# Optimization experiments

Hardware: AMD Instinct MI355X
Metric: run time of the kernel (lower is better)

Reference implementation:

```python
import jax, jax.numpy as jnp
import numpy as np

B, C, H, W = 32, 64, 64, 64
OC = 2 * C  # same_c=False -> out_channels = 2*in_channels


def _conv(x, w, b, stride):
    y = jax.lax.conv_general_dilated(
        x, w, (stride, stride), ((1, 1), (1, 1)),
        dimension_numbers=('NCHW', 'OIHW', 'NCHW'))
    return y + b[None, :, None, None]


def _lrelu(x):
    return jnp.where(x >= 0, x, 0.1 * x)


def _roi_align_full(x, ph, pw, sr=2):
    # torchvision RoIAlign, aligned=False, spatial_scale=1, sampling_ratio=2,
    # single ROI per batch item covering [0, 0, W-1, H-1].
    b, c, h, w = x.shape
    bin_h = max(float(h - 1), 1.0) / ph
    bin_w = max(float(w - 1), 1.0) / pw
    off = (jnp.arange(sr, dtype=jnp.float32) + 0.5) / sr
    ys = ((jnp.arange(ph, dtype=jnp.float32)[:, None] + off[None, :]).reshape(-1) * bin_h)  # [ph*sr]
    xs = ((jnp.arange(pw, dtype=jnp.float32)[:, None] + off[None, :]).reshape(-1) * bin_w)  # [pw*sr]
    y0 = jnp.floor(ys).astype(jnp.int32)
    x0 = jnp.floor(xs).astype(jnp.int32)
    y1 = jnp.minimum(y0 + 1, h - 1)
    x1 = jnp.minimum(x0 + 1, w - 1)
    ly = ys - y0.astype(jnp.float32); hy = 1.0 - ly
    lx = xs - x0.astype(jnp.float32); hx = 1.0 - lx
    # gather 4 bilinear corners: [B, C, ph*sr, pw*sr]
    v00 = x[:, :, y0][:, :, :, x0]
    v01 = x[:, :, y0][:, :, :, x1]
    v10 = x[:, :, y1][:, :, :, x0]
    v11 = x[:, :, y1][:, :, :, x1]
    val = (hy[:, None] * hx[None, :]) * v00 + (hy[:, None] * lx[None, :]) * v01 \
        + (ly[:, None] * hx[None, :]) * v10 + (ly[:, None] * lx[None, :]) * v11
    # average the sr x sr samples per bin
    return val.reshape(b, c, ph, sr, pw, sr).mean(axis=(3, 5))


def setup_inputs() -> dict:
    key = jax.random.key(0)
    ks = jax.random.split(key, 20)
    def p(k, shape):
        return jax.random.normal(k, shape, dtype=jnp.float32) * 0.05
    return {
        'out1': jax.random.normal(ks[0], (B, C, H, W), dtype=jnp.float32),
        'out2': jax.random.normal(ks[1], (B, C, H, W), dtype=jnp.float32),
        'out3': jax.random.normal(ks[2], (B, C, H, W), dtype=jnp.float32),
        'w1': p(ks[3], (OC, C, 3, 3)),      'b1': p(ks[4], (OC,)),
        'w2': p(ks[5], (OC, OC, 3, 3)),     'b2': p(ks[6], (OC,)),
        'w3': p(ks[7], (OC, OC, 3, 3)),     'b3': p(ks[8], (OC,)),
        'w_aux': p(ks[9], (OC, OC, 3, 3)),  'b_aux': p(ks[10], (OC,)),
        'w_b2': p(ks[11], (OC, 2 * OC, 3, 3)), 'b_b2': p(ks[12], (OC,)),
        'w_prev': p(ks[13], (OC, 2 * C, 3, 3)), 'b_prev': p(ks[14], (OC,)),
        'lin_w': p(ks[15], (H * W, C)),     'lin_b': p(ks[16], (H * W,)),
    }


def reference(out1, out2, out3, w1, b1, w2, b2, w3, b3,
              w_aux, b_aux, w_b2, b_b2, w_prev, b_prev, lin_w, lin_b):
    bsz, c, h, w = out1.shape
    l1 = _lrelu(_conv(out1, w1, b1, 1))
    l2 = _lrelu(_conv(l1, w2, b2, 1))
    l3 = _lrelu(_conv(l2, w3, b3, 1))
    roi1 = _roi_align_full(l2, h // 2, w // 2)
    aux = _lrelu(_conv(l3, w_aux, b_aux, 2))        # dropout = identity (eval)
    block_out1 = roi1 + aux
    block_out2 = _lrelu(_conv(jnp.concatenate([l1, l2], axis=1), w_b2, b_b2, 2))
    prev = _lrelu(_conv(jnp.concatenate([out2, out3], axis=1), w_prev, b_prev, 1))
    # fused per-pixel attention: logits[b,p] = <lin_w[p], out1[b,:,p]> + lin_b[p]
    xp = out1.reshape(bsz, c, h * w)                 # [B, C, P], P row-major over (h, w)
    logits = jnp.einsum('bcp,pc->bp', xp, lin_w) + lin_b
    attn = jax.nn.softmax(logits, axis=-1).reshape(bsz, 1, h, w)
    block_out3 = _roi_align_full(prev * attn, h // 2, w // 2)
    return jnp.stack([block_out1 + block_out2 + block_out3, block_out2, block_out3])
```

## Files before the change

### kernel.cpp

```cpp
#include <hip/hip_runtime.h>
#include <hip/hip_bf16.h>

typedef __attribute__((ext_vector_type(8))) short short8;
typedef __attribute__((ext_vector_type(4))) float f32x4;

constexpr int B = 32, C = 64, HW = 4096;

__device__ __forceinline__ unsigned short f2bf(float f) {
    __hip_bfloat16 h = __float2bfloat16(f);
    unsigned short u; __builtin_memcpy(&u, &h, 2); return u;
}
__device__ __forceinline__ float b2f(unsigned short u) {
    unsigned int t = ((unsigned int)u) << 16; float f; __builtin_memcpy(&f, &t, 4); return f;
}
__device__ __forceinline__ void gllds16(const void* g, void* l) {
    __builtin_amdgcn_global_load_lds((const __attribute__((address_space(1))) unsigned int*)g,
                                     (__attribute__((address_space(3))) unsigned int*)l, 16, 0, 0);
}

__global__ __launch_bounds__(256) void tr_k(const float* __restrict__ out1,
                                            const float* __restrict__ out2,
                                            const float* __restrict__ out3,
                                            unsigned short* __restrict__ t1,
                                            unsigned short* __restrict__ tp)
{
    int t = threadIdx.x;
    int px = blockIdx.x * 256 + t;
    int b = blockIdx.y;
    if (blockIdx.z == 0) {
        const float* src = out1 + (size_t)b * 64 * HW + px;
        unsigned short v[64];
#pragma unroll
        for (int c = 0; c < 64; ++c) v[c] = f2bf(src[(size_t)c * HW]);
        unsigned short* dst = t1 + ((size_t)b * HW + px) * 64;
#pragma unroll
        for (int j = 0; j < 8; ++j)
            *(short8*)(dst + j * 8) = *(short8*)(v + j * 8);
    } else {
        const float* s2 = out2 + (size_t)b * 64 * HW + px;
        const float* s3 = out3 + (size_t)b * 64 * HW + px;
        unsigned short v[128];
#pragma unroll
        for (int c = 0; c < 64; ++c) v[c] = f2bf(s2[(size_t)c * HW]);
#pragma unroll
        for (int c = 0; c < 64; ++c) v[64 + c] = f2bf(s3[(size_t)c * HW]);
        unsigned short* dst = tp + ((size_t)b * HW + px) * 128;
#pragma unroll
        for (int j = 0; j < 16; ++j)
            *(short8*)(dst + j * 8) = *(short8*)(v + j * 8);
    }
}

__global__ __launch_bounds__(256) void logits_k(const float* __restrict__ out1,
                                                const float* __restrict__ lin_w,
                                                const float* __restrict__ lin_b,
                                                float* __restrict__ logits)
{
    int b = blockIdx.x >> 4;
    int p = (blockIdx.x & 15) * 256 + threadIdx.x;
    float acc = lin_b[p];
    const float* xb = out1 + (size_t)b * C * HW + p;
    const float* wp = lin_w + (size_t)p * C;
#pragma unroll
    for (int c = 0; c < C; c += 4) {
        float4 w4 = *(const float4*)(wp + c);
        acc = fmaf(xb[(size_t)c * HW],       w4.x, acc);
        acc = fmaf(xb[(size_t)(c + 1) * HW], w4.y, acc);
        acc = fmaf(xb[(size_t)(c + 2) * HW], w4.z, acc);
        acc = fmaf(xb[(size_t)(c + 3) * HW], w4.w, acc);
    }
    logits[(size_t)b * HW + p] = acc;
}

__global__ __launch_bounds__(256) void softmax_k(const float* __restrict__ logits,
                                                 float* __restrict__ attn)
{
    int b = blockIdx.x, tid = threadIdx.x;
    float lg[16];
#pragma unroll
    for (int k = 0; k < 16; ++k) lg[k] = logits[(size_t)b * HW + tid + (k << 8)];
    __shared__ float red[256];
    float m = -INFINITY;
#pragma unroll
    for (int k = 0; k < 16; ++k) m = fmaxf(m, lg[k]);
    red[tid] = m; __syncthreads();
    for (int s = 128; s > 0; s >>= 1) {
        if (tid < s) red[tid] = fmaxf(red[tid], red[tid + s]);
        __syncthreads();
    }
    m = red[0]; __syncthreads();
    float se = 0.f;
#pragma unroll
    for (int k = 0; k < 16; ++k) { lg[k] = __expf(lg[k] - m); se += lg[k]; }
    red[tid] = se; __syncthreads();
    for (int s = 128; s > 0; s >>= 1) {
        if (tid < s) red[tid] += red[tid + s];
        __syncthreads();
    }
    float inv = 1.0f / red[0];
#pragma unroll
    for (int k = 0; k < 16; ++k)
        attn[(size_t)b * HW + tid + (k << 8)] = lg[k] * inv;
}

__global__ __launch_bounds__(256) void wprep_k(const float* w1, const float* w2, const float* w3,
                                               const float* wa, const float* wb2, const float* wp,
                                               unsigned short* __restrict__ wT)
{
    int blk = blockIdx.x;
    int base, ic, l2ic, off; const float* src;
    if      (blk < 32)  { base = 0;   ic = 64;  l2ic = 6; off = 0;      src = w1;  }
    else if (blk < 96)  { base = 32;  ic = 128; l2ic = 7; off = 73728;  src = w2;  }
    else if (blk < 160) { base = 96;  ic = 128; l2ic = 7; off = 221184; src = w3;  }
    else if (blk < 224) { base = 160; ic = 128; l2ic = 7; off = 368640; src = wa;  }
    else if (blk < 352) { base = 224; ic = 256; l2ic = 8; off = 516096; src = wb2; }
    else                { base = 352; ic = 128; l2ic = 7; off = 811008; src = wp;  }
    int pair = (blk - base) * 256 + threadIdx.x;
    int oc = pair >> l2ic, icx = pair & (ic - 1);
    const float* s = src + ((size_t)(oc * ic + icx)) * 9;
#pragma unroll
    for (int k = 0; k < 9; ++k)
        wT[(size_t)off + ((size_t)(k * 128 + oc)) * ic + icx] = f2bf(s[k]);
}

template<int IC, int STRIDE, int PS_IN, int CO_IN, int OPS, int OCO, bool ATTN>
__global__ __launch_bounds__(256, 4) void conv_k(
    const unsigned short* __restrict__ in,
    const unsigned short* __restrict__ wTc,
    const float* __restrict__ bias,
    const float* __restrict__ attn,
    unsigned short* __restrict__ out)
{
    constexpr int NICG = IC / 32;
    constexpr int L = (IC == 64) ? 1 : (IC == 128) ? 2 : 3;
    constexpr int NS = 9 * NICG;
    constexpr int NPX = (STRIDE == 1) ? 4096 : 1024;
    constexpr int WO = (STRIDE == 1) ? 64 : 32;

    __shared__ char bsm[2][8192];

    int t = threadIdx.x;
    int wave = t >> 6, lane = t & 63;
    int mw = wave & 1, nw = wave >> 1;
    int l15 = lane & 15, lc = lane >> 4;
    int y0 = blockIdx.x, b = blockIdx.y;

    int bofs[4];
#pragma unroll
    for (int nf = 0; nf < 4; ++nf) {
        int oc = nw * 64 + nf * 16 + l15;
        bofs[nf] = oc * 64 + ((lc ^ ((oc >> 1) & 3)) << 4);
    }
    int oc0 = t >> 2;
    int c0 = (t & 3) ^ ((oc0 >> 1) & 3);
    const unsigned short* wsrc = wTc + oc0 * IC + c0 * 8;
    char* lbase = &bsm[0][0] + (wave << 10);

    const unsigned short* base_b = in + (size_t)b * HW * PS_IN + CO_IN + (lc << 3);
    int col[2];
#pragma unroll
    for (int f = 0; f < 2; ++f)
        col[f] = (STRIDE == 1) ? (mw * 32 + f * 16 + l15) : (f * 16 + l15);

    f32x4 acc[2][4];
#pragma unroll
    for (int f = 0; f < 2; ++f)
#pragma unroll
        for (int nf = 0; nf < 4; ++nf) acc[f][nf] = (f32x4)0.0f;

    auto stage = [&](int s, int buf) {
        int kk = s >> L, icg = s & (NICG - 1);
        const unsigned short* p = wsrc + (size_t)kk * 128 * IC + icg * 32;
        char* d = lbase + buf * 8192;
        gllds16(p, d);
        gllds16(p + 64 * IC, d + 4096);
    };

    stage(0, 0);
    __syncthreads();

    for (int s = 0; s < NS; ++s) {
        int cur = s & 1;
        if (s + 1 < NS) stage(s + 1, cur ^ 1);
        int kk = s >> L, icg = s & (NICG - 1);
        int ky = (kk * 11) >> 5;
        int kx = kk - ky * 3;
        int iy = (STRIDE == 1) ? (y0 + ky - 1) : ((y0 * 2 + mw) * 2 + ky - 1);
        bool yok = (unsigned)iy < 64u;
        const unsigned short* prow = base_b + (long)iy * (64 * PS_IN) + icg * 32;
        short8 az = {0, 0, 0, 0, 0, 0, 0, 0};
        short8 aa[2];
#pragma unroll
        for (int f = 0; f < 2; ++f) {
            int ix = (STRIDE == 1) ? (col[f] + kx - 1) : (2 * col[f] + kx - 1);
            bool ok = yok && ((unsigned)ix < 64u);
            const short8* ap = (const short8*)(prow + (long)ix * PS_IN);
            aa[f] = ok ? *ap : az;
        }
        const char* bb_base = &bsm[0][0] + cur * 8192;
        short8 bb[4];
#pragma unroll
        for (int nf = 0; nf < 4; ++nf)
            bb[nf] = *(const short8*)(bb_base + bofs[nf]);
#pragma unroll
        for (int f = 0; f < 2; ++f)
#pragma unroll
            for (int nf = 0; nf < 4; ++nf)
                acc[f][nf] = __builtin_amdgcn_mfma_f32_16x16x32_bf16(aa[f], bb[nf], acc[f][nf], 0, 0, 0);
        __syncthreads();
    }

    int orow = (STRIDE == 1) ? y0 : (y0 * 2 + mw);
    float bs[4];
#pragma unroll
    for (int nf = 0; nf < 4; ++nf) bs[nf] = bias[nw * 64 + nf * 16 + l15];
#pragma unroll
    for (int f = 0; f < 2; ++f) {
#pragma unroll
        for (int r = 0; r < 4; ++r) {
            int pxcol = ((STRIDE == 1) ? mw * 32 : 0) + f * 16 + (lc << 2) + r;
            float av = 1.0f;
            if constexpr (ATTN) av = attn[(size_t)b * HW + y0 * 64 + pxcol];
            size_t obase = ((size_t)b * NPX + (size_t)orow * WO + pxcol) * OPS + OCO;
#pragma unroll
            for (int nf = 0; nf < 4; ++nf) {
                int oc = nw * 64 + nf * 16 + l15;
                float v = acc[f][nf][r] + bs[nf];
                v = (v >= 0.0f) ? v : 0.1f * v;
                if constexpr (ATTN) v *= av;
                out[obase + oc] = f2bf(v);
            }
        }
    }
}

__device__ __forceinline__ void acc8(float* a, const unsigned short* p, float w) {
    short8 v = *(const short8*)p;
#pragma unroll
    for (int k = 0; k < 8; ++k) a[k] = fmaf(w, b2f((unsigned short)v[k]), a[k]);
}

__global__ __launch_bounds__(256) void fuse_roi_k(const unsigned short* __restrict__ prevs,
                                                  const unsigned short* __restrict__ l12,
                                                  const unsigned short* __restrict__ auxb,
                                                  const unsigned short* __restrict__ bo2b,
                                                  float* __restrict__ o0,
                                                  float* __restrict__ o1,
                                                  float* __restrict__ o2)
{
    int idx = blockIdx.x * 256 + threadIdx.x;
    int j = idx & 31, i = (idx >> 5) & 31, ocg = (idx >> 10) & 15, b = idx >> 14;
    float a3[8] = {0,0,0,0,0,0,0,0}, aR[8] = {0,0,0,0,0,0,0,0};
    const unsigned short* pb = prevs + (size_t)b * HW * 128 + ocg * 8;
    const unsigned short* lb = l12 + (size_t)b * HW * 256 + 128 + ocg * 8;
#pragma unroll
    for (int sy = 0; sy < 2; ++sy) {
        float ys = (i + 0.25f + 0.5f * sy) * 1.96875f;
        int y0 = (int)ys;
        int y1 = min(y0 + 1, 63);
        float ly = ys - (float)y0, hy = 1.0f - ly;
#pragma unroll
        for (int sx = 0; sx < 2; ++sx) {
            float xs = (j + 0.25f + 0.5f * sx) * 1.96875f;
            int x0 = (int)xs;
            int x1 = min(x0 + 1, 63);
            float lx = xs - (float)x0, hx = 1.0f - lx;
            int p00 = y0 * 64 + x0, p01 = y0 * 64 + x1, p10 = y1 * 64 + x0, p11 = y1 * 64 + x1;
            float w00 = hy * hx, w01 = hy * lx, w10 = ly * hx, w11 = ly * lx;
            acc8(a3, pb + (size_t)p00 * 128, w00); acc8(a3, pb + (size_t)p01 * 128, w01);
            acc8(a3, pb + (size_t)p10 * 128, w10); acc8(a3, pb + (size_t)p11 * 128, w11);
            acc8(aR, lb + (size_t)p00 * 256, w00); acc8(aR, lb + (size_t)p01 * 256, w01);
            acc8(aR, lb + (size_t)p10 * 256, w10); acc8(aR, lb + (size_t)p11 * 256, w11);
        }
    }
    int p32 = i * 32 + j;
    const unsigned short* ax = auxb + ((size_t)(b * 1024 + p32)) * 128 + ocg * 8;
    const unsigned short* b2 = bo2b + ((size_t)(b * 1024 + p32)) * 128 + ocg * 8;
#pragma unroll
    for (int k = 0; k < 8; ++k) {
        int oc = ocg * 8 + k;
        size_t ob = ((size_t)(b * 128 + oc)) * 1024 + p32;
        float v3 = a3[k] * 0.25f;
        float v2 = b2f(b2[k]);
        o2[ob] = v3;
        o1[ob] = v2;
        o0[ob] = aR[k] * 0.25f + b2f(ax[k]) + v2 + v3;
    }
}

extern "C" void kernel_launch(void* const* d_in, const int* in_sizes, int n_in,
                              void* d_out, int out_size, void* d_ws, size_t ws_size,
                              hipStream_t stream)
{
    const float* out1  = (const float*)d_in[0];
    const float* out2  = (const float*)d_in[1];
    const float* out3  = (const float*)d_in[2];
    const float* w1    = (const float*)d_in[3];  const float* b1    = (const float*)d_in[4];
    const float* w2    = (const float*)d_in[5];  const float* b2    = (const float*)d_in[6];
    const float* w3    = (const float*)d_in[7];  const float* b3    = (const float*)d_in[8];
    const float* w_aux = (const float*)d_in[9];  const float* b_aux = (const float*)d_in[10];
    const float* w_b2  = (const float*)d_in[11]; const float* b_b2  = (const float*)d_in[12];
    const float* w_prev= (const float*)d_in[13]; const float* b_prev= (const float*)d_in[14];
    const float* lin_w = (const float*)d_in[15]; const float* lin_b = (const float*)d_in[16];

    char* ws = (char*)d_ws;
    unsigned short* l12cat = (unsigned short*)(ws);
    unsigned short* l3     = (unsigned short*)(ws + 67108864);
    unsigned short* prevs  = l3;
    unsigned short* auxb   = (unsigned short*)(ws + 100663296);
    unsigned short* bo2b   = (unsigned short*)(ws + 109051904);
    float* attn   = (float*)(ws + 117440512);
    float* logits = (float*)(ws + 117964800);
    unsigned short* wT = (unsigned short*)(ws + 118489088);

    unsigned short* t1 = (unsigned short*)d_out;
    unsigned short* tp = t1 + (size_t)B * HW * 64;

    float* o0 = (float*)d_out;
    float* o1 = o0 + (size_t)B * 128 * 1024;
    float* o2 = o1 + (size_t)B * 128 * 1024;

    wprep_k<<<dim3(416), dim3(256), 0, stream>>>(w1, w2, w3, w_aux, w_b2, w_prev, wT);
    tr_k<<<dim3(16, B, 2), dim3(256), 0, stream>>>(out1, out2, out3, t1, tp);
    logits_k<<<dim3(B * 16), dim3(256), 0, stream>>>(out1, lin_w, lin_b, logits);
    softmax_k<<<dim3(B), dim3(256), 0, stream>>>(logits, attn);

    conv_k<64, 1, 64, 0, 256, 0, false><<<dim3(64, B), dim3(256), 0, stream>>>(
        t1, wT + 0, b1, nullptr, l12cat);
    conv_k<128, 1, 256, 0, 256, 128, false><<<dim3(64, B), dim3(256), 0, stream>>>(
        l12cat, wT + 73728, b2, nullptr, l12cat);
    conv_k<128, 1, 256, 128, 128, 0, false><<<dim3(64, B), dim3(256), 0, stream>>>(
        l12cat, wT + 221184, b3, nullptr, l3);
    conv_k<128, 2, 128, 0, 128, 0, false><<<dim3(16, B), dim3(256), 0, stream>>>(
        l3, wT + 368640, b_aux, nullptr, auxb);
    conv_k<256, 2, 256, 0, 128, 0, false><<<dim3(16, B), dim3(256), 0, stream>>>(
        l12cat, wT + 516096, b_b2, nullptr, bo2b);
    conv_k<128, 1, 128, 0, 128, 0, true><<<dim3(64, B), dim3(256), 0, stream>>>(
        tp, wT + 811008, b_prev, attn, prevs);

    fuse_roi_k<<<dim3(2048), dim3(256), 0, stream>>>(prevs, l12cat, auxb, bo2b, o0, o1, o2);
}
```

Baseline: 686.0 us.

## Software-pipeline conv A-operand loads and fuse logits into transpose kernel

The conv kernel's main loop now prefetches the next step's activation fragments into registers alongside the next weight tile. It unrolls by two with ping-pong register sets and replaces the full __syncthreads with an explicit vmcnt wait plus s_barrier, so global latency overlaps the MFMAs. Separately, the attention logits dot product moves into the transpose kernel, which already reads out1, removing one kernel launch and a second full read of out1. The manual waitcnt relies on the count of outstanding loads; the s+=2 unroll assumes NS is even, which holds since NS=9*NICG with NICG even.

```diff
diff --git a/kernel.cpp b/kernel.cpp
--- a/kernel.cpp
+++ b/kernel.cpp
@@ -17,25 +17,43 @@
     __builtin_amdgcn_global_load_lds((const __attribute__((address_space(1))) unsigned int*)g,
                                      (__attribute__((address_space(3))) unsigned int*)l, 16, 0, 0);
 }
+__device__ __forceinline__ void cfence() { asm volatile("" ::: "memory"); }
+__device__ __forceinline__ void vmcnt2() { asm volatile("s_waitcnt vmcnt(2)" ::: "memory"); }
+__device__ __forceinline__ void vmcnt0() { asm volatile("s_waitcnt vmcnt(0)" ::: "memory"); }
 
 __global__ __launch_bounds__(256) void tr_k(const float* __restrict__ out1,
                                             const float* __restrict__ out2,
                                             const float* __restrict__ out3,
+                                            const float* __restrict__ lin_w,
+                                            const float* __restrict__ lin_b,
                                             unsigned short* __restrict__ t1,
-                                            unsigned short* __restrict__ tp)
+                                            unsigned short* __restrict__ tp,
+                                            float* __restrict__ logits)
 {
     int t = threadIdx.x;
     int px = blockIdx.x * 256 + t;
     int b = blockIdx.y;
     if (blockIdx.z == 0) {
         const float* src = out1 + (size_t)b * 64 * HW + px;
+        const float* lwp = lin_w + (size_t)px * 64;
+        float acc = lin_b[px];
         unsigned short v[64];
 #pragma unroll
-        for (int c = 0; c < 64; ++c) v[c] = f2bf(src[(size_t)c * HW]);
+        for (int c = 0; c < 64; c += 4) {
+            float4 w4 = *(const float4*)(lwp + c);
+            float x0 = src[(size_t)c * HW];
+            float x1 = src[(size_t)(c + 1) * HW];
+            float x2 = src[(size_t)(c + 2) * HW];
+            float x3 = src[(size_t)(c + 3) * HW];
+            acc = fmaf(x0, w4.x, acc); acc = fmaf(x1, w4.y, acc);
+            acc = fmaf(x2, w4.z, acc); acc = fmaf(x3, w4.w, acc);
+            v[c] = f2bf(x0); v[c + 1] = f2bf(x1); v[c + 2] = f2bf(x2); v[c + 3] = f2bf(x3);
+        }
         unsigned short* dst = t1 + ((size_t)b * HW + px) * 64;
 #pragma unroll
         for (int j = 0; j < 8; ++j)
             *(short8*)(dst + j * 8) = *(short8*)(v + j * 8);
+        logits[(size_t)b * HW + px] = acc;
     } else {
         const float* s2 = out2 + (size_t)b * 64 * HW + px;
         const float* s3 = out3 + (size_t)b * 64 * HW + px;
@@ -49,27 +67,6 @@
         for (int j = 0; j < 16; ++j)
             *(short8*)(dst + j * 8) = *(short8*)(v + j * 8);
     }
-}
-
-__global__ __launch_bounds__(256) void logits_k(const float* __restrict__ out1,
-                                                const float* __restrict__ lin_w,
-                                                const float* __restrict__ lin_b,
-                                                float* __restrict__ logits)
-{
-    int b = blockIdx.x >> 4;
-    int p = (blockIdx.x & 15) * 256 + threadIdx.x;
-    float acc = lin_b[p];
-    const float* xb = out1 + (size_t)b * C * HW + p;
-    const float* wp = lin_w + (size_t)p * C;
-#pragma unroll
-    for (int c = 0; c < C; c += 4) {
-        float4 w4 = *(const float4*)(wp + c);
-        acc = fmaf(xb[(size_t)c * HW],       w4.x, acc);
-        acc = fmaf(xb[(size_t)(c + 1) * HW], w4.y, acc);
-        acc = fmaf(xb[(size_t)(c + 2) * HW], w4.z, acc);
-        acc = fmaf(xb[(size_t)(c + 3) * HW], w4.w, acc);
-    }
-    logits[(size_t)b * HW + p] = acc;
 }
 
 __global__ __launch_bounds__(256) void softmax_k(const float* __restrict__ logits,
@@ -132,7 +129,7 @@
     unsigned short* __restrict__ out)
 {
     constexpr int NICG = IC / 32;
-    constexpr int L = (IC == 64) ? 1 : (IC == 128) ? 2 : 3;
+    constexpr int LG = (IC == 64) ? 1 : (IC == 128) ? 2 : 3;
     constexpr int NS = 9 * NICG;
     constexpr int NPX = (STRIDE == 1) ? 4096 : 1024;
     constexpr int WO = (STRIDE == 1) ? 64 : 32;
@@ -162,6 +159,8 @@
     for (int f = 0; f < 2; ++f)
         col[f] = (STRIDE == 1) ? (mw * 32 + f * 16 + l15) : (f * 16 + l15);
 
+    const short8 zero8 = {0, 0, 0, 0, 0, 0, 0, 0};
+
     f32x4 acc[2][4];
 #pragma unroll
     for (int f = 0; f < 2; ++f)
@@ -169,33 +168,34 @@
         for (int nf = 0; nf < 4; ++nf) acc[f][nf] = (f32x4)0.0f;
 
     auto stage = [&](int s, int buf) {
-        int kk = s >> L, icg = s & (NICG - 1);
+        int kk = s >> LG, icg = s & (NICG - 1);
         const unsigned short* p = wsrc + (size_t)kk * 128 * IC + icg * 32;
         char* d = lbase + buf * 8192;
         gllds16(p, d);
         gllds16(p + 64 * IC, d + 4096);
     };
-
-    stage(0, 0);
-    __syncthreads();
-
-    for (int s = 0; s < NS; ++s) {
-        int cur = s & 1;
-        if (s + 1 < NS) stage(s + 1, cur ^ 1);
-        int kk = s >> L, icg = s & (NICG - 1);
+    auto loadA = [&](int s, short8& d0, short8& d1) {
+        int kk = s >> LG, icg = s & (NICG - 1);
         int ky = (kk * 11) >> 5;
         int kx = kk - ky * 3;
         int iy = (STRIDE == 1) ? (y0 + ky - 1) : ((y0 * 2 + mw) * 2 + ky - 1);
         bool yok = (unsigned)iy < 64u;
         const unsigned short* prow = base_b + (long)iy * (64 * PS_IN) + icg * 32;
-        short8 az = {0, 0, 0, 0, 0, 0, 0, 0};
-        short8 aa[2];
 #pragma unroll
         for (int f = 0; f < 2; ++f) {
             int ix = (STRIDE == 1) ? (col[f] + kx - 1) : (2 * col[f] + kx - 1);
             bool ok = yok && ((unsigned)ix < 64u);
             const short8* ap = (const short8*)(prow + (long)ix * PS_IN);
-            aa[f] = ok ? *ap : az;
+            short8 v = ok ? *ap : zero8;
+            if (f == 0) d0 = v; else d1 = v;
+        }
+    };
+    auto body = [&](int s, int cur, short8& Ac0, short8& Ac1, short8& An0, short8& An1) {
+        bool more = (s + 1 < NS);
+        if (more) {
+            stage(s + 1, cur ^ 1);
+            cfence();
+            loadA(s + 1, An0, An1);
         }
         const char* bb_base = &bsm[0][0] + cur * 8192;
         short8 bb[4];
@@ -203,11 +203,25 @@
         for (int nf = 0; nf < 4; ++nf)
             bb[nf] = *(const short8*)(bb_base + bofs[nf]);
 #pragma unroll
-        for (int f = 0; f < 2; ++f)
-#pragma unroll
-            for (int nf = 0; nf < 4; ++nf)
-                acc[f][nf] = __builtin_amdgcn_mfma_f32_16x16x32_bf16(aa[f], bb[nf], acc[f][nf], 0, 0, 0);
-        __syncthreads();
+        for (int nf = 0; nf < 4; ++nf) {
+            acc[0][nf] = __builtin_amdgcn_mfma_f32_16x16x32_bf16(Ac0, bb[nf], acc[0][nf], 0, 0, 0);
+            acc[1][nf] = __builtin_amdgcn_mfma_f32_16x16x32_bf16(Ac1, bb[nf], acc[1][nf], 0, 0, 0);
+        }
+        if (more) {
+            vmcnt2();
+            __builtin_amdgcn_s_barrier();
+        }
+    };
+
+    short8 Aa0, Aa1, Ab0, Ab1;
+    stage(0, 0);
+    loadA(0, Aa0, Aa1);
+    vmcnt0();
+    __builtin_amdgcn_s_barrier();
+
+    for (int s = 0; s < NS; s += 2) {
+        body(s,     0, Aa0, Aa1, Ab0, Ab1);
+        body(s + 1, 1, Ab0, Ab1, Aa0, Aa1);
     }
 
     int orow = (STRIDE == 1) ? y0 : (y0 * 2 + mw);
@@ -321,8 +335,7 @@
     float* o2 = o1 + (size_t)B * 128 * 1024;
 
     wprep_k<<<dim3(416), dim3(256), 0, stream>>>(w1, w2, w3, w_aux, w_b2, w_prev, wT);
-    tr_k<<<dim3(16, B, 2), dim3(256), 0, stream>>>(out1, out2, out3, t1, tp);
-    logits_k<<<dim3(B * 16), dim3(256), 0, stream>>>(out1, lin_w, lin_b, logits);
+    tr_k<<<dim3(16, B, 2), dim3(256), 0, stream>>>(out1, out2, out3, lin_w, lin_b, t1, tp, logits);
     softmax_k<<<dim3(B), dim3(256), 0, stream>>>(logits, attn);
 
     conv_k<64, 1, 64, 0, 256, 0, false><<<dim3(64, B), dim3(256), 0, stream>>>(
```

Result: faster. 659.7 us (-3.8%).
